# Kernel optimization log

Hardware: AMD Instinct MI355X
Metric: run time of the kernel (lower is better)

Reference implementation:

```python
import jax, jax.numpy as jnp
import numpy as np

ALPHA = 0.2      # LeakyReLU negative slope
NEG = -9e15     # mask fill value, as in pyGAT

B, N, NFEAT, NHID, NCLASS, NHEADS = 4, 2048, 128, 64, 32, 8


def setup_inputs() -> dict:
    key = jax.random.key(0)
    ks = jax.random.split(key, 8)
    x = jax.random.normal(ks[0], (B, N, NFEAT), dtype=jnp.float32)
    adj = jax.random.randint(ks[1], (B, N, N), 0, 2, dtype=jnp.int32)
    W = jax.random.normal(ks[2], (NHEADS, NFEAT, NHID), dtype=jnp.float32) * 0.1
    a1 = jax.random.normal(ks[3], (NHEADS, NHID), dtype=jnp.float32) * 0.1
    a2 = jax.random.normal(ks[4], (NHEADS, NHID), dtype=jnp.float32) * 0.1
    Wo = jax.random.normal(ks[5], (NHEADS * NHID, NCLASS), dtype=jnp.float32) * 0.1
    ao1 = jax.random.normal(ks[6], (NCLASS,), dtype=jnp.float32) * 0.1
    ao2 = jax.random.normal(ks[7], (NCLASS,), dtype=jnp.float32) * 0.1
    return {"x": x, "adj": adj, "W": W, "a1": a1, "a2": a2,
            "Wo": Wo, "ao1": ao1, "ao2": ao2}


def _gat_forward(x, adj, W, a1, a2, Wo, ao1, ao2):
    mask = adj > 0  # [B, N, N]
    # --- multi-head layer (concat=True) ---
    Wh = jnp.einsum('bnf,hfd->bhnd', x, W)          # [B,H,N,nhid]
    f1 = jnp.einsum('bhnd,hd->bhn', Wh, a1)          # Wh @ a[:nhid]
    f2 = jnp.einsum('bhnd,hd->bhn', Wh, a2)          # Wh @ a[nhid:]
    e = jax.nn.leaky_relu(f1[..., :, None] + f2[..., None, :], ALPHA)
    att = jax.nn.softmax(jnp.where(mask[:, None], e, NEG), axis=-1)
    h = jax.nn.elu(jnp.einsum('bhnm,bhmd->bhnd', att, Wh))  # [B,H,N,nhid]
    # torch.cat along dim=2: [B, N, H*nhid]
    h = jnp.transpose(h, (0, 2, 1, 3)).reshape(B, N, NHEADS * NHID)
    # (dropout layers are no-ops in eval mode)
    # --- output head (concat=False, no ELU) ---
    Wh2 = jnp.einsum('bnf,fc->bnc', h, Wo)           # [B,N,nclass]
    g1 = jnp.einsum('bnc,c->bn', Wh2, ao1)
    g2 = jnp.einsum('bnc,c->bn', Wh2, ao2)
    e2 = jax.nn.leaky_relu(g1[:, :, None] + g2[:, None, :], ALPHA)
    att2 = jax.nn.softmax(jnp.where(mask, e2, NEG), axis=-1)
    return jnp.einsum('bnm,bmc->bnc', att2, Wh2)     # [B,N,nclass]


def reference(x, adj, W, a1, a2, Wo, ao1, ao2):
    return _gat_forward(x, adj, W, a1, a2, Wo, ao1, ao2)
```

## Files before the change

kernel.cpp:

```cpp
#include <hip/hip_runtime.h>


typedef short  short8  __attribute__((ext_vector_type(8)));
typedef float  float4_ __attribute__((ext_vector_type(4)));
typedef float  float2_ __attribute__((ext_vector_type(2)));
typedef unsigned int uint4_ __attribute__((ext_vector_type(4)));

#if __has_builtin(__builtin_amdgcn_exp2f)
#define EXP2(x) __builtin_amdgcn_exp2f(x)
#else
#define EXP2(x) __expf((x) * 0.69314718055994531f)
#endif
#define LOG2E 1.44269504088896340f

static __device__ __forceinline__ unsigned short f2bf(float f) {
  unsigned u = __float_as_uint(f);
  u += 0x7fffu + ((u >> 16) & 1u);
  return (unsigned short)(u >> 16);
}
static __device__ __forceinline__ unsigned pk2bf(float a, float b) {
  return (unsigned)f2bf(a) | ((unsigned)f2bf(b) << 16);
}
static __device__ __forceinline__ unsigned upack(float s) {
  return ((unsigned)f2bf(EXP2(0.2f * s)) << 16) | f2bf(EXP2(s));
}

static __device__ __forceinline__ unsigned bitm(unsigned mb, int jj) {
#if __has_builtin(__builtin_amdgcn_sbfe)
  return (unsigned)__builtin_amdgcn_sbfe((int)mb, jj, 1);
#else
  return 0u - ((mb >> jj) & 1u);
#endif
}

static __device__ __forceinline__ unsigned wmax2(unsigned w0, unsigned w1,
    unsigned m0, unsigned m1, float2_ Av, float2_ A2v) {
  float2_ lo = {__uint_as_float(w0 << 16), __uint_as_float(w1 << 16)};
  float2_ hi = {__uint_as_float(w0 & 0xFFFF0000u), __uint_as_float(w1 & 0xFFFF0000u)};
  float2_ p = Av * lo;
  float2_ n = A2v * hi;
  float2_ m = __builtin_elementwise_max(p, n);
  unsigned e0 = __float_as_uint(m.x) & m0;
  unsigned e1 = __float_as_uint(m.y) & m1;
  return __builtin_amdgcn_perm(e1, e0, 0x07060302u);
}

__global__ __launch_bounds__(256) void k_wfrag(
    const float* __restrict__ Wm, const float* __restrict__ Wo,
    short* __restrict__ Wf, short* __restrict__ WoF) {
  if (blockIdx.x < 32) {
    const int T = blockIdx.x * 256 + threadIdx.x;
    const int lane = T & 63;
    int r = T >> 6;
    const int nt = r & 3; r >>= 2;
    const int kstep = r & 3; r >>= 2;
    const int h = r;
    const int kk = kstep * 32 + (lane >> 4) * 8;
    const int n = nt * 16 + (lane & 15);
    const float* sp = Wm + h * 8192 + kk * 64 + n;
    short8 o;
    #pragma unroll
    for (int jj = 0; jj < 8; ++jj) o[jj] = (short)f2bf(sp[jj * 64]);
    *(short8*)(Wf + T * 8) = o;
  } else {
    const int T = (blockIdx.x - 32) * 256 + threadIdx.x;
    const int lane = T & 63;
    const int nt = (T >> 6) & 1, kstep = T >> 7;
    const int kk = kstep * 32 + (lane >> 4) * 8;
    const int n = nt * 16 + (lane & 15);
    short8 o;
    #pragma unroll
    for (int jj = 0; jj < 8; ++jj) o[jj] = (short)f2bf(Wo[(kk + jj) * 32 + n]);
    *(short8*)(WoF + T * 8) = o;
  }
}

__global__ __launch_bounds__(256) void k_front(
    const int* __restrict__ adj, unsigned long long* __restrict__ maskb,
    const float* __restrict__ x, const short* __restrict__ Wf,
    const float* __restrict__ a1, const float* __restrict__ a2,
    short* __restrict__ WhF, float* __restrict__ f1, unsigned* __restrict__ f2p) {
  __shared__ float wsm[64 * 68];
  const int bx = blockIdx.x;
  const int t = threadIdx.x;
  if (bx >= 1024) {
    const int lane = t & 63, wid = t >> 6;
    const int s = lane & 15;
    const long long row0 = (long long)(bx - 1024) * 4;
    for (int rr = 0; rr < 4; ++rr) {
      const long long row = row0 + rr;
      const int4* src = (const int4*)(adj + row * 2048);
      #pragma unroll
      for (int c = 0; c < 2; ++c) {
        int4 v = src[c * 256 + t];
        unsigned nib = (v.x != 0 ? 1u : 0u) | (v.y != 0 ? 2u : 0u) |
                       (v.z != 0 ? 4u : 0u) | (v.w != 0 ? 8u : 0u);
        unsigned lo = (s < 8) ? (nib << (s * 4)) : 0u;
        unsigned hi = (s >= 8) ? (nib << ((s - 8) * 4)) : 0u;
        #pragma unroll
        for (int off = 1; off < 16; off <<= 1) {
          lo |= __shfl_xor(lo, off);
          hi |= __shfl_xor(hi, off);
        }
        if (s == 0) {
          int word = c * 16 + wid * 4 + (lane >> 4);
          maskb[row * 32 + word] = ((unsigned long long)hi << 32) | (unsigned long long)lo;
        }
      }
    }
    return;
  }
  const int itile = bx & 31, bh = bx >> 5;
  const int b = bh >> 3, h = bh & 7;
  const int i0 = itile * 64;
  const int lane = t & 63, w = t >> 6;
  const int cl = lane & 15, q = lane >> 4;
  const float* xrow = x + ((long long)b * 2048 + i0 + w * 16 + cl) * 128;
  const short* wfh = Wf + h * 8192;
  float4_ acc0 = {0.f, 0.f, 0.f, 0.f}, acc1 = acc0, acc2 = acc0, acc3 = acc0;
  #pragma unroll
  for (int kstep = 0; kstep < 4; ++kstep) {
    const float* xp = xrow + kstep * 32 + q * 8;
    const float4 xa = *(const float4*)xp;
    const float4 xb = *(const float4*)(xp + 4);
    uint4_ ap;
    ap.x = pk2bf(xa.x, xa.y);
    ap.y = pk2bf(xa.z, xa.w);
    ap.z = pk2bf(xb.x, xb.y);
    ap.w = pk2bf(xb.z, xb.w);
    const short8 af = __builtin_bit_cast(short8, ap);
    const short* bp = wfh + kstep * 2048 + lane * 8;
    const short8 b0 = *(const short8*)(bp);
    const short8 b1 = *(const short8*)(bp + 512);
    const short8 b2 = *(const short8*)(bp + 1024);
    const short8 b3 = *(const short8*)(bp + 1536);
    acc0 = __builtin_amdgcn_mfma_f32_16x16x32_bf16(af, b0, acc0, 0, 0, 0);
    acc1 = __builtin_amdgcn_mfma_f32_16x16x32_bf16(af, b1, acc1, 0, 0, 0);
    acc2 = __builtin_amdgcn_mfma_f32_16x16x32_bf16(af, b2, acc2, 0, 0, 0);
    acc3 = __builtin_amdgcn_mfma_f32_16x16x32_bf16(af, b3, acc3, 0, 0, 0);
  }
  {
    float4_ accs[4] = {acc0, acc1, acc2, acc3};
    #pragma unroll
    for (int nt = 0; nt < 4; ++nt)
      #pragma unroll
      for (int reg = 0; reg < 4; ++reg)
        wsm[(w * 16 + q * 4 + reg) * 68 + nt * 16 + cl] = accs[nt][reg];
  }
  __syncthreads();
  {
    const int row = t >> 2, seg = t & 3;
    const float* wr = wsm + row * 68 + seg * 16;
    const float4* a1p = (const float4*)(a1 + h * 64 + seg * 16);
    const float4* a2p = (const float4*)(a2 + h * 64 + seg * 16);
    float p1 = 0.f, p2 = 0.f;
    #pragma unroll
    for (int u = 0; u < 4; ++u) {
      const float4 wv = *(const float4*)(wr + u * 4);
      const float4 v1 = a1p[u];
      const float4 v2 = a2p[u];
      p1 += wv.x * v1.x + wv.y * v1.y + wv.z * v1.z + wv.w * v1.w;
      p2 += wv.x * v2.x + wv.y * v2.y + wv.z * v2.z + wv.w * v2.w;
    }
    p1 += __shfl_xor(p1, 1); p1 += __shfl_xor(p1, 2);
    p2 += __shfl_xor(p2, 1); p2 += __shfl_xor(p2, 2);
    if (seg == 0) {
      f1[(long long)bh * 2048 + i0 + row] = p1 * LOG2E;
      f2p[(long long)bh * 2048 + i0 + row] = upack(p2 * LOG2E);
    }
  }
  #pragma unroll
  for (int u = 0; u < 2; ++u) {
    const int idx = u * 256 + t;
    const int l2 = idx & 63, nt2 = (idx >> 6) & 3, ks2 = idx >> 8;
    const int jrow = ks2 * 32 + (l2 >> 4) * 8;
    const int d = nt2 * 16 + (l2 & 15);
    short8 o;
    #pragma unroll
    for (int jj = 0; jj < 8; ++jj) o[jj] = (short)f2bf(wsm[(jrow + jj) * 68 + d]);
    const long long off = (long long)bh * 131072 + (long long)itile * 4096 +
                          ks2 * 2048 + nt2 * 512 + l2 * 8;
    *(short8*)(WhF + off) = o;
  }
}

__global__ __launch_bounds__(256) void k_attn1(
    const short* __restrict__ whf, const float* __restrict__ f1v,
    const unsigned* __restrict__ f2pv, const unsigned long long* __restrict__ maskb,
    short* __restrict__ hA) {
  __shared__ short bsm[2][8192];
  __shared__ unsigned f2s[2048];
  const int bh = blockIdx.y, b = bh >> 3, hh = bh & 7;
  const int t = threadIdx.x;
  const int lane = t & 63, wid = t >> 6;
  const int cl = lane & 15, q = lane >> 4;
  const long long i_g = (long long)blockIdx.x * 64 + wid * 16 + cl;
  const float f1i = f1v[(long long)bh * 2048 + i_g];
  const float A = EXP2(f1i), A2 = EXP2(0.2f * f1i);
  const float2_ Av = {A, A}, A2v = {A2, A2};
  const uint2* mpp = (const uint2*)(maskb + ((long long)b * 2048 + i_g) * 32);
  const unsigned* f2b = f2pv + (long long)bh * 2048;
  const short* whfb = whf + (long long)bh * 131072;
  const float4* gB = (const float4*)whfb;
  const short8 vones = {16256, 16256, 16256, 16256, 16256, 16256, 16256, 16256};
  ((uint4_*)f2s)[t] = ((const uint4_*)f2b)[t];
  ((uint4_*)f2s)[256 + t] = ((const uint4_*)f2b)[256 + t];
  {
    float4 st0[4];
    #pragma unroll
    for (int u = 0; u < 4; ++u) st0[u] = gB[u * 256 + t];
    #pragma unroll
    for (int u = 0; u < 4; ++u) ((float4*)bsm[0])[u * 256 + t] = st0[u];
  }
  uint2 mw0_c = mpp[0], mw1_c = mpp[1];
  float4_ acc0 = {0.f, 0.f, 0.f, 0.f}, acc1 = acc0, acc2 = acc0, acc3 = acc0;
  float4_ accz = acc0;
  const int qs = q * 8;
  for (int s = 0; s < 16; ++s) {
    float4 stn0, stn1, stn2, stn3;
    if (s < 15) {
      const float4* gp = gB + (s + 1) * 1024 + t;
      stn0 = gp[0]; stn1 = gp[256]; stn2 = gp[512]; stn3 = gp[768];
    }
    const uint2 mwA = mw0_c, mwB = mw1_c;
    if (s < 15) { mw0_c = mpp[s * 2 + 2]; mw1_c = mpp[s * 2 + 3]; }
    __syncthreads();
    const short* bsb = bsm[s & 1] + lane * 8;
    #pragma unroll
    for (int jc2 = 0; jc2 < 2; ++jc2) {
      const int jc = s * 2 + jc2;
      const uint2 mw = jc2 ? mwB : mwA;
      #pragma unroll
      for (int ks = 0; ks < 2; ++ks) {
        const unsigned mb = (ks ? mw.y : mw.x) >> qs;
        const unsigned* up = f2s + jc * 64 + ks * 32 + qs;
        const uint4_ wa = *(const uint4_*)up;
        const uint4_ wb = *(const uint4_*)(up + 4);
        uint4_ pk;
        pk.x = wmax2(wa.x, wa.y, bitm(mb, 0), bitm(mb, 1), Av, A2v);
        pk.y = wmax2(wa.z, wa.w, bitm(mb, 2), bitm(mb, 3), Av, A2v);
        pk.z = wmax2(wb.x, wb.y, bitm(mb, 4), bitm(mb, 5), Av, A2v);
        pk.w = wmax2(wb.z, wb.w, bitm(mb, 6), bitm(mb, 7), Av, A2v);
        const short8 af = __builtin_bit_cast(short8, pk);
        const short* bp = bsb + (jc2 * 2 + ks) * 2048;
        short8 b0 = *(const short8*)(bp);
        short8 b1 = *(const short8*)(bp + 512);
        short8 b2 = *(const short8*)(bp + 1024);
        short8 b3 = *(const short8*)(bp + 1536);
        acc0 = __builtin_amdgcn_mfma_f32_16x16x32_bf16(af, b0, acc0, 0, 0, 0);
        acc1 = __builtin_amdgcn_mfma_f32_16x16x32_bf16(af, b1, acc1, 0, 0, 0);
        acc2 = __builtin_amdgcn_mfma_f32_16x16x32_bf16(af, b2, acc2, 0, 0, 0);
        acc3 = __builtin_amdgcn_mfma_f32_16x16x32_bf16(af, b3, acc3, 0, 0, 0);
        accz = __builtin_amdgcn_mfma_f32_16x16x32_bf16(af, vones, accz, 0, 0, 0);
      }
    }
    if (s < 15) {
      float4* dp = (float4*)bsm[(s + 1) & 1] + t;
      dp[0] = stn0; dp[256] = stn1; dp[512] = stn2; dp[768] = stn3;
    }
  }
  __syncthreads();
  float* hs = (float*)bsm;
  {
    float4_ accs[4] = {acc0, acc1, acc2, acc3};
    #pragma unroll
    for (int reg = 0; reg < 4; ++reg) {
      const float rz = 1.f / accz[reg];
      #pragma unroll
      for (int nt = 0; nt < 4; ++nt) {
        float v = accs[nt][reg] * rz;
        v = (v > 0.f) ? v : (__expf(v) - 1.f);
        hs[(wid * 16 + q * 4 + reg) * 68 + nt * 16 + cl] = v;
      }
    }
  }
  __syncthreads();
  const int rtg0 = b * 128 + blockIdx.x * 4;
  #pragma unroll
  for (int u = 0; u < 2; ++u) {
    const int id = u * 256 + t;
    const int l2 = id & 63, ks2 = (id >> 6) & 1, rtile = id >> 7;
    const int rowl = rtile * 16 + (l2 & 15);
    const int d = ks2 * 32 + (l2 >> 4) * 8;
    const float* hp = hs + rowl * 68 + d;
    const float4 va = *(const float4*)hp;
    const float4 vb = *(const float4*)(hp + 4);
    uint4_ o;
    o.x = pk2bf(va.x, va.y); o.y = pk2bf(va.z, va.w);
    o.z = pk2bf(vb.x, vb.y); o.w = pk2bf(vb.z, vb.w);
    const long long rt = rtg0 + rtile;
    const int kstep = hh * 2 + ks2;
    *(uint4_*)(hA + ((rt * 16 + kstep) * 64 + l2) * 8) = o;
  }
}

__global__ __launch_bounds__(128) void k_ogemm(
    const short* __restrict__ hA, const short* __restrict__ WoF,
    const float* __restrict__ ao1, const float* __restrict__ ao2,
    short* __restrict__ Wh2F, float* __restrict__ g1, unsigned* __restrict__ g2p) {
  __shared__ float w2s[32 * 36];
  const int t = threadIdx.x, lane = t & 63, wv = t >> 6;
  const int cl = lane & 15, q = lane >> 4;
  const long long rt = (long long)blockIdx.x * 2 + wv;
  float4_ acc0 = {0.f, 0.f, 0.f, 0.f}, acc1 = acc0;
  const short* ap = hA + rt * 8192 + lane * 8;
  const short* bp = WoF + lane * 8;
  #pragma unroll
  for (int kstep = 0; kstep < 16; ++kstep) {
    const short8 af = *(const short8*)(ap + kstep * 512);
    const short8 b0 = *(const short8*)(bp + kstep * 1024);
    const short8 b1 = *(const short8*)(bp + kstep * 1024 + 512);
    acc0 = __builtin_amdgcn_mfma_f32_16x16x32_bf16(af, b0, acc0, 0, 0, 0);
    acc1 = __builtin_amdgcn_mfma_f32_16x16x32_bf16(af, b1, acc1, 0, 0, 0);
  }
  const float o1a = ao1[cl], o1b = ao1[cl + 16];
  const float o2a = ao2[cl], o2b = ao2[cl + 16];
  #pragma unroll
  for (int reg = 0; reg < 4; ++reg) {
    const int rowl = wv * 16 + q * 4 + reg;
    w2s[rowl * 36 + cl] = acc0[reg];
    w2s[rowl * 36 + 16 + cl] = acc1[reg];
    float p1 = acc0[reg] * o1a + acc1[reg] * o1b;
    float p2 = acc0[reg] * o2a + acc1[reg] * o2b;
    p1 += __shfl_xor(p1, 1); p1 += __shfl_xor(p1, 2);
    p1 += __shfl_xor(p1, 4); p1 += __shfl_xor(p1, 8);
    p2 += __shfl_xor(p2, 1); p2 += __shfl_xor(p2, 2);
    p2 += __shfl_xor(p2, 4); p2 += __shfl_xor(p2, 8);
    if (cl == 0) {
      const long long row = (long long)blockIdx.x * 32 + rowl;
      g1[row] = p1 * LOG2E;
      g2p[row] = upack(p2 * LOG2E);
    }
  }
  __syncthreads();
  {
    const int l2 = t & 63, nt2 = t >> 6;
    const int g = blockIdx.x >> 6, jc = (blockIdx.x >> 1) & 31, ks2 = blockIdx.x & 1;
    const int kb = (l2 >> 4) * 8, n = nt2 * 16 + (l2 & 15);
    short8 o;
    #pragma unroll
    for (int jj = 0; jj < 8; ++jj) o[jj] = (short)f2bf(w2s[(kb + jj) * 36 + n]);
    const long long off = (long long)g * 65536 + jc * 2048 + ks2 * 1024 +
                          nt2 * 512 + l2 * 8;
    *(short8*)(Wh2F + off) = o;
  }
}

__global__ __launch_bounds__(256) void k_attn2(
    const short* __restrict__ whf2, const float* __restrict__ g1v,
    const unsigned* __restrict__ g2pv, const unsigned long long* __restrict__ maskb,
    float* __restrict__ outp) {
  __shared__ float accs[4][16][33];
  __shared__ float zsh[64];
  const int b = blockIdx.y;
  const long long i0 = (long long)blockIdx.x * 16;
  const int t = threadIdx.x, lane = t & 63, wid = t >> 6;
  const int cl = lane & 15, q = lane >> 4;
  const float g1i = g1v[(long long)b * 2048 + i0 + cl];
  const float A = EXP2(g1i), A2 = EXP2(0.2f * g1i);
  const float2_ Av = {A, A}, A2v = {A2, A2};
  const uint2* mpp = (const uint2*)(maskb + ((long long)b * 2048 + i0 + cl) * 32);
  const unsigned* g2b = g2pv + (long long)b * 2048;
  const short* wb = whf2 + (long long)b * 65536;
  const short8 vones = {16256, 16256, 16256, 16256, 16256, 16256, 16256, 16256};
  float4_ acc0 = {0.f, 0.f, 0.f, 0.f}, acc1 = acc0, accz = acc0;
  const int qs = q * 8;
  const int jc0 = wid * 8;
  uint2 mw_c = mpp[jc0];
  uint4_ wa0_c = *(const uint4_*)(g2b + jc0 * 64 + qs);
  uint4_ wb0_c = *(const uint4_*)(g2b + jc0 * 64 + qs + 4);
  uint4_ wa1_c = *(const uint4_*)(g2b + jc0 * 64 + 32 + qs);
  uint4_ wb1_c = *(const uint4_*)(g2b + jc0 * 64 + 36 + qs);
  for (int c8 = 0; c8 < 8; ++c8) {
    const int jc = jc0 + c8;
    const uint2 mw = mw_c;
    const uint4_ wa0 = wa0_c, wb0 = wb0_c, wa1 = wa1_c, wb1 = wb1_c;
    {
      const int jn = jc + ((c8 < 7) ? 1 : 0);
      const unsigned* fp = g2b + jn * 64 + qs;
      mw_c = mpp[jn];
      wa0_c = *(const uint4_*)fp;
      wb0_c = *(const uint4_*)(fp + 4);
      wa1_c = *(const uint4_*)(fp + 32);
      wb1_c = *(const uint4_*)(fp + 36);
    }
    const short* bb = wb + (jc * 2) * 1024 + lane * 8;
    {
      const unsigned mb = mw.x >> qs;
      uint4_ pk;
      pk.x = wmax2(wa0.x, wa0.y, bitm(mb, 0), bitm(mb, 1), Av, A2v);
      pk.y = wmax2(wa0.z, wa0.w, bitm(mb, 2), bitm(mb, 3), Av, A2v);
      pk.z = wmax2(wb0.x, wb0.y, bitm(mb, 4), bitm(mb, 5), Av, A2v);
      pk.w = wmax2(wb0.z, wb0.w, bitm(mb, 6), bitm(mb, 7), Av, A2v);
      const short8 af = __builtin_bit_cast(short8, pk);
      short8 b0 = *(const short8*)bb;
      short8 b1 = *(const short8*)(bb + 512);
      acc0 = __builtin_amdgcn_mfma_f32_16x16x32_bf16(af, b0, acc0, 0, 0, 0);
      acc1 = __builtin_amdgcn_mfma_f32_16x16x32_bf16(af, b1, acc1, 0, 0, 0);
      accz = __builtin_amdgcn_mfma_f32_16x16x32_bf16(af, vones, accz, 0, 0, 0);
    }
    {
      const unsigned mb = mw.y >> qs;
      uint4_ pk;
      pk.x = wmax2(wa1.x, wa1.y, bitm(mb, 0), bitm(mb, 1), Av, A2v);
      pk.y = wmax2(wa1.z, wa1.w, bitm(mb, 2), bitm(mb, 3), Av, A2v);
      pk.z = wmax2(wb1.x, wb1.y, bitm(mb, 4), bitm(mb, 5), Av, A2v);
      pk.w = wmax2(wb1.z, wb1.w, bitm(mb, 6), bitm(mb, 7), Av, A2v);
      const short8 af = __builtin_bit_cast(short8, pk);
      const short* bk = bb + 1024;
      short8 b0 = *(const short8*)bk;
      short8 b1 = *(const short8*)(bk + 512);
      acc0 = __builtin_amdgcn_mfma_f32_16x16x32_bf16(af, b0, acc0, 0, 0, 0);
      acc1 = __builtin_amdgcn_mfma_f32_16x16x32_bf16(af, b1, acc1, 0, 0, 0);
      accz = __builtin_amdgcn_mfma_f32_16x16x32_bf16(af, vones, accz, 0, 0, 0);
    }
  }
  if (cl == 0) {
    #pragma unroll
    for (int reg = 0; reg < 4; ++reg) zsh[wid * 16 + q * 4 + reg] = accz[reg];
  }
  float4_ a01[2] = {acc0, acc1};
  #pragma unroll
  for (int nt = 0; nt < 2; ++nt)
    #pragma unroll
    for (int reg = 0; reg < 4; ++reg)
      accs[wid][q * 4 + reg][nt * 16 + cl] = a01[nt][reg];
  __syncthreads();
  #pragma unroll
  for (int r = 0; r < 2; ++r) {
    int o = r * 256 + t;
    int il = o >> 5, c = o & 31;
    float s = accs[0][il][c] + accs[1][il][c] + accs[2][il][c] + accs[3][il][c];
    float Z = zsh[il] + zsh[16 + il] + zsh[32 + il] + zsh[48 + il];
    outp[((long long)b * 2048 + i0 + il) * 32 + c] = s / Z;
  }
}

extern "C" void kernel_launch(void* const* d_in, const int* in_sizes, int n_in,
                              void* d_out, int out_size, void* d_ws, size_t ws_size,
                              hipStream_t stream) {
  const float* x   = (const float*)d_in[0];
  const int*   adj = (const int*)d_in[1];
  const float* W   = (const float*)d_in[2];
  const float* a1  = (const float*)d_in[3];
  const float* a2  = (const float*)d_in[4];
  const float* Wo  = (const float*)d_in[5];
  const float* ao1 = (const float*)d_in[6];
  const float* ao2 = (const float*)d_in[7];
  float* out = (float*)d_out;
  char* ws = (char*)d_ws;

  unsigned long long* maskb = (unsigned long long*)(ws + 0);
  short* Wf   = (short*)(ws + 2097152);
  short* WoF  = (short*)(ws + 2228224);
  short* WhF  = (short*)(ws + 18874368);
  float* f1   = (float*)(ws + 27262976);
  unsigned* f2p = (unsigned*)(ws + 27525120);
  short* hA   = (short*)(ws + 27787264);
  short* Wh2F = (short*)(ws + 45613056);
  float* g1   = (float*)(ws + 46137344);
  unsigned* g2p = (unsigned*)(ws + 46170112);

  hipLaunchKernelGGL(k_wfrag, dim3(40), dim3(256), 0, stream, W, Wo, Wf, WoF);
  hipLaunchKernelGGL(k_front, dim3(3072), dim3(256), 0, stream, adj, maskb,
                     x, Wf, a1, a2, WhF, f1, f2p);
  hipLaunchKernelGGL(k_attn1, dim3(32, 32), dim3(256), 0, stream, WhF, f1, f2p, maskb, hA);
  hipLaunchKernelGGL(k_ogemm, dim3(256), dim3(128), 0, stream, hA, WoF, ao1, ao2,
                     Wh2F, g1, g2p);
  hipLaunchKernelGGL(k_attn2, dim3(128, 4), dim3(256), 0, stream, Wh2F, g1, g2p, maskb, out);
}
```

Baseline: 181.0 us.

## Switch attention layer-1 to 32x32x16 MFMA with split-K across wave pairs

Rewrites k_attn1 so each wave computes a 32-row tile with 32x32x16 bf16 MFMAs instead of 16x16x32. Waves are split into two row groups and two key halves, and the partial sums are reduced through shared memory. The WhF fragment layout and the f2 exponent storage (now separate U/U2 bf16 arrays) are changed to match the new operand layout. ELU and normalization move into the final pack stage. This cuts the MFMA count and the row-sum overhead per output, at the cost of an extra LDS reduction and sync.

```diff
diff --git a/kernel.cpp b/kernel.cpp
--- a/kernel.cpp
+++ b/kernel.cpp
@@ -4,6 +4,7 @@
 typedef short  short8  __attribute__((ext_vector_type(8)));
 typedef float  float4_ __attribute__((ext_vector_type(4)));
 typedef float  float2_ __attribute__((ext_vector_type(2)));
+typedef float  float16_ __attribute__((ext_vector_type(16)));
 typedef unsigned int uint4_ __attribute__((ext_vector_type(4)));
 
 #if __has_builtin(__builtin_amdgcn_exp2f)
@@ -39,6 +40,18 @@
   float2_ hi = {__uint_as_float(w0 & 0xFFFF0000u), __uint_as_float(w1 & 0xFFFF0000u)};
   float2_ p = Av * lo;
   float2_ n = A2v * hi;
+  float2_ m = __builtin_elementwise_max(p, n);
+  unsigned e0 = __float_as_uint(m.x) & m0;
+  unsigned e1 = __float_as_uint(m.y) & m1;
+  return __builtin_amdgcn_perm(e1, e0, 0x07060302u);
+}
+
+static __device__ __forceinline__ unsigned wmax2u(unsigned uw, unsigned u2w,
+    unsigned m0, unsigned m1, float2_ Av, float2_ A2v) {
+  float2_ Uf  = {__uint_as_float(uw << 16),  __uint_as_float(uw & 0xFFFF0000u)};
+  float2_ U2f = {__uint_as_float(u2w << 16), __uint_as_float(u2w & 0xFFFF0000u)};
+  float2_ p = Av * Uf;
+  float2_ n = A2v * U2f;
   float2_ m = __builtin_elementwise_max(p, n);
   unsigned e0 = __float_as_uint(m.x) & m0;
   unsigned e1 = __float_as_uint(m.y) & m1;
@@ -79,7 +92,8 @@
     const int* __restrict__ adj, unsigned long long* __restrict__ maskb,
     const float* __restrict__ x, const short* __restrict__ Wf,
     const float* __restrict__ a1, const float* __restrict__ a2,
-    short* __restrict__ WhF, float* __restrict__ f1, unsigned* __restrict__ f2p) {
+    short* __restrict__ WhF, float* __restrict__ f1,
+    unsigned short* __restrict__ Uv, unsigned short* __restrict__ U2v) {
   __shared__ float wsm[64 * 68];
   const int bx = blockIdx.x;
   const int t = threadIdx.x;
@@ -166,45 +180,46 @@
     p2 += __shfl_xor(p2, 1); p2 += __shfl_xor(p2, 2);
     if (seg == 0) {
       f1[(long long)bh * 2048 + i0 + row] = p1 * LOG2E;
-      f2p[(long long)bh * 2048 + i0 + row] = upack(p2 * LOG2E);
+      const float s2 = p2 * LOG2E;
+      Uv[(long long)bh * 2048 + i0 + row] = f2bf(EXP2(s2));
+      U2v[(long long)bh * 2048 + i0 + row] = f2bf(EXP2(0.2f * s2));
     }
   }
   #pragma unroll
   for (int u = 0; u < 2; ++u) {
     const int idx = u * 256 + t;
-    const int l2 = idx & 63, nt2 = (idx >> 6) & 3, ks2 = idx >> 8;
-    const int jrow = ks2 * 32 + (l2 >> 4) * 8;
-    const int d = nt2 * 16 + (l2 & 15);
+    const int l2 = idx & 63, dtile = (idx >> 6) & 1, win = (idx >> 7) & 1, ks2 = idx >> 8;
+    const int jloc = ks2 * 32 + win * 16 + (l2 >> 5) * 8;
+    const int d = dtile * 32 + (l2 & 31);
     short8 o;
     #pragma unroll
-    for (int jj = 0; jj < 8; ++jj) o[jj] = (short)f2bf(wsm[(jrow + jj) * 68 + d]);
+    for (int jj = 0; jj < 8; ++jj) o[jj] = (short)f2bf(wsm[(jloc + jj) * 68 + d]);
     const long long off = (long long)bh * 131072 + (long long)itile * 4096 +
-                          ks2 * 2048 + nt2 * 512 + l2 * 8;
+                          ks2 * 2048 + win * 1024 + dtile * 512 + l2 * 8;
     *(short8*)(WhF + off) = o;
   }
 }
 
 __global__ __launch_bounds__(256) void k_attn1(
     const short* __restrict__ whf, const float* __restrict__ f1v,
-    const unsigned* __restrict__ f2pv, const unsigned long long* __restrict__ maskb,
-    short* __restrict__ hA) {
+    const unsigned short* __restrict__ Uv, const unsigned short* __restrict__ U2v,
+    const unsigned* __restrict__ mask32, short* __restrict__ hA) {
   __shared__ short bsm[2][8192];
-  __shared__ unsigned f2s[2048];
+  __shared__ unsigned short Us[2048], U2s[2048];
   const int bh = blockIdx.y, b = bh >> 3, hh = bh & 7;
-  const int t = threadIdx.x;
-  const int lane = t & 63, wid = t >> 6;
-  const int cl = lane & 15, q = lane >> 4;
-  const long long i_g = (long long)blockIdx.x * 64 + wid * 16 + cl;
+  const int t = threadIdx.x, lane = t & 63, wid = t >> 6;
+  const int rg = wid & 1, jh = wid >> 1;
+  const int m = lane & 31, hi8 = lane >> 5;
+  const long long i_g = (long long)blockIdx.x * 64 + rg * 32 + m;
   const float f1i = f1v[(long long)bh * 2048 + i_g];
   const float A = EXP2(f1i), A2 = EXP2(0.2f * f1i);
   const float2_ Av = {A, A}, A2v = {A2, A2};
-  const uint2* mpp = (const uint2*)(maskb + ((long long)b * 2048 + i_g) * 32);
-  const unsigned* f2b = f2pv + (long long)bh * 2048;
+  const unsigned* mp = mask32 + ((long long)b * 2048 + i_g) * 64 + jh;
   const short* whfb = whf + (long long)bh * 131072;
   const float4* gB = (const float4*)whfb;
   const short8 vones = {16256, 16256, 16256, 16256, 16256, 16256, 16256, 16256};
-  ((uint4_*)f2s)[t] = ((const uint4_*)f2b)[t];
-  ((uint4_*)f2s)[256 + t] = ((const uint4_*)f2b)[256 + t];
+  ((uint4_*)Us)[t]  = ((const uint4_*)(Uv  + (long long)bh * 2048))[t];
+  ((uint4_*)U2s)[t] = ((const uint4_*)(U2v + (long long)bh * 2048))[t];
   {
     float4 st0[4];
     #pragma unroll
@@ -212,46 +227,41 @@
     #pragma unroll
     for (int u = 0; u < 4; ++u) ((float4*)bsm[0])[u * 256 + t] = st0[u];
   }
-  uint2 mw0_c = mpp[0], mw1_c = mpp[1];
-  float4_ acc0 = {0.f, 0.f, 0.f, 0.f}, acc1 = acc0, acc2 = acc0, acc3 = acc0;
-  float4_ accz = acc0;
-  const int qs = q * 8;
+  unsigned mw0_c = mp[0], mw1_c = mp[2];
+  float16_ acc0 = {0.f,0.f,0.f,0.f,0.f,0.f,0.f,0.f,0.f,0.f,0.f,0.f,0.f,0.f,0.f,0.f};
+  float16_ acc1 = acc0, accz = acc0;
+  const int uoff = jh * 32 + hi8 * 8;
   for (int s = 0; s < 16; ++s) {
     float4 stn0, stn1, stn2, stn3;
     if (s < 15) {
       const float4* gp = gB + (s + 1) * 1024 + t;
       stn0 = gp[0]; stn1 = gp[256]; stn2 = gp[512]; stn3 = gp[768];
     }
-    const uint2 mwA = mw0_c, mwB = mw1_c;
-    if (s < 15) { mw0_c = mpp[s * 2 + 2]; mw1_c = mpp[s * 2 + 3]; }
+    const unsigned mwA = mw0_c, mwB = mw1_c;
+    if (s < 15) { mw0_c = mp[(s * 2 + 2) * 2]; mw1_c = mp[(s * 2 + 3) * 2]; }
     __syncthreads();
-    const short* bsb = bsm[s & 1] + lane * 8;
+    const short* bsb = bsm[s & 1];
     #pragma unroll
     for (int jc2 = 0; jc2 < 2; ++jc2) {
       const int jc = s * 2 + jc2;
-      const uint2 mw = jc2 ? mwB : mwA;
+      const unsigned mword = jc2 ? mwB : mwA;
       #pragma unroll
-      for (int ks = 0; ks < 2; ++ks) {
-        const unsigned mb = (ks ? mw.y : mw.x) >> qs;
-        const unsigned* up = f2s + jc * 64 + ks * 32 + qs;
-        const uint4_ wa = *(const uint4_*)up;
-        const uint4_ wb = *(const uint4_*)(up + 4);
+      for (int win = 0; win < 2; ++win) {
+        const unsigned mb = mword >> (win * 16 + hi8 * 8);
+        const uint4_ uv  = *(const uint4_*)(Us  + jc * 64 + uoff + win * 16);
+        const uint4_ u2v = *(const uint4_*)(U2s + jc * 64 + uoff + win * 16);
         uint4_ pk;
-        pk.x = wmax2(wa.x, wa.y, bitm(mb, 0), bitm(mb, 1), Av, A2v);
-        pk.y = wmax2(wa.z, wa.w, bitm(mb, 2), bitm(mb, 3), Av, A2v);
-        pk.z = wmax2(wb.x, wb.y, bitm(mb, 4), bitm(mb, 5), Av, A2v);
-        pk.w = wmax2(wb.z, wb.w, bitm(mb, 6), bitm(mb, 7), Av, A2v);
+        pk.x = wmax2u(uv.x, u2v.x, bitm(mb, 0), bitm(mb, 1), Av, A2v);
+        pk.y = wmax2u(uv.y, u2v.y, bitm(mb, 2), bitm(mb, 3), Av, A2v);
+        pk.z = wmax2u(uv.z, u2v.z, bitm(mb, 4), bitm(mb, 5), Av, A2v);
+        pk.w = wmax2u(uv.w, u2v.w, bitm(mb, 6), bitm(mb, 7), Av, A2v);
         const short8 af = __builtin_bit_cast(short8, pk);
-        const short* bp = bsb + (jc2 * 2 + ks) * 2048;
-        short8 b0 = *(const short8*)(bp);
-        short8 b1 = *(const short8*)(bp + 512);
-        short8 b2 = *(const short8*)(bp + 1024);
-        short8 b3 = *(const short8*)(bp + 1536);
-        acc0 = __builtin_amdgcn_mfma_f32_16x16x32_bf16(af, b0, acc0, 0, 0, 0);
-        acc1 = __builtin_amdgcn_mfma_f32_16x16x32_bf16(af, b1, acc1, 0, 0, 0);
-        acc2 = __builtin_amdgcn_mfma_f32_16x16x32_bf16(af, b2, acc2, 0, 0, 0);
-        acc3 = __builtin_amdgcn_mfma_f32_16x16x32_bf16(af, b3, acc3, 0, 0, 0);
-        accz = __builtin_amdgcn_mfma_f32_16x16x32_bf16(af, vones, accz, 0, 0, 0);
+        const short* bp = bsb + jc2 * 4096 + jh * 2048 + win * 1024 + lane * 8;
+        const short8 b0 = *(const short8*)bp;
+        const short8 b1 = *(const short8*)(bp + 512);
+        acc0 = __builtin_amdgcn_mfma_f32_32x32x16_bf16(af, b0, acc0, 0, 0, 0);
+        acc1 = __builtin_amdgcn_mfma_f32_32x32x16_bf16(af, b1, acc1, 0, 0, 0);
+        accz = __builtin_amdgcn_mfma_f32_32x32x16_bf16(af, vones, accz, 0, 0, 0);
       }
     }
     if (s < 15) {
@@ -261,17 +271,32 @@
   }
   __syncthreads();
   float* hs = (float*)bsm;
-  {
-    float4_ accs[4] = {acc0, acc1, acc2, acc3};
-    #pragma unroll
-    for (int reg = 0; reg < 4; ++reg) {
-      const float rz = 1.f / accz[reg];
+  float* zs = hs + 64 * 68;
+  if (jh == 0) {
+    #pragma unroll
+    for (int r = 0; r < 16; ++r) {
+      const int rowl = rg * 32 + (r & 3) + 8 * (r >> 2) + 4 * hi8;
+      hs[rowl * 68 + m] = acc0[r];
+      hs[rowl * 68 + 32 + m] = acc1[r];
+    }
+    if (m == 0) {
       #pragma unroll
-      for (int nt = 0; nt < 4; ++nt) {
-        float v = accs[nt][reg] * rz;
-        v = (v > 0.f) ? v : (__expf(v) - 1.f);
-        hs[(wid * 16 + q * 4 + reg) * 68 + nt * 16 + cl] = v;
-      }
+      for (int r = 0; r < 16; ++r)
+        zs[rg * 32 + (r & 3) + 8 * (r >> 2) + 4 * hi8] = accz[r];
+    }
+  }
+  __syncthreads();
+  if (jh == 1) {
+    #pragma unroll
+    for (int r = 0; r < 16; ++r) {
+      const int rowl = rg * 32 + (r & 3) + 8 * (r >> 2) + 4 * hi8;
+      hs[rowl * 68 + m] += acc0[r];
+      hs[rowl * 68 + 32 + m] += acc1[r];
+    }
+    if (m == 0) {
+      #pragma unroll
+      for (int r = 0; r < 16; ++r)
+        zs[rg * 32 + (r & 3) + 8 * (r >> 2) + 4 * hi8] += accz[r];
     }
   }
   __syncthreads();
@@ -282,12 +307,17 @@
     const int l2 = id & 63, ks2 = (id >> 6) & 1, rtile = id >> 7;
     const int rowl = rtile * 16 + (l2 & 15);
     const int d = ks2 * 32 + (l2 >> 4) * 8;
+    const float rz = 1.f / zs[rowl];
     const float* hp = hs + rowl * 68 + d;
-    const float4 va = *(const float4*)hp;
-    const float4 vb = *(const float4*)(hp + 4);
+    float v[8];
+    #pragma unroll
+    for (int k = 0; k < 8; ++k) {
+      float x = hp[k] * rz;
+      v[k] = (x > 0.f) ? x : (__expf(x) - 1.f);
+    }
     uint4_ o;
-    o.x = pk2bf(va.x, va.y); o.y = pk2bf(va.z, va.w);
-    o.z = pk2bf(vb.x, vb.y); o.w = pk2bf(vb.z, vb.w);
+    o.x = pk2bf(v[0], v[1]); o.y = pk2bf(v[2], v[3]);
+    o.z = pk2bf(v[4], v[5]); o.w = pk2bf(v[6], v[7]);
     const long long rt = rtg0 + rtile;
     const int kstep = hh * 2 + ks2;
     *(uint4_*)(hA + ((rt * 16 + kstep) * 64 + l2) * 8) = o;
@@ -455,7 +485,8 @@
   short* WoF  = (short*)(ws + 2228224);
   short* WhF  = (short*)(ws + 18874368);
   float* f1   = (float*)(ws + 27262976);
-  unsigned* f2p = (unsigned*)(ws + 27525120);
+  unsigned short* Uv  = (unsigned short*)(ws + 27525120);
+  unsigned short* U2v = (unsigned short*)(ws + 27656192);
   short* hA   = (short*)(ws + 27787264);
   short* Wh2F = (short*)(ws + 45613056);
   float* g1   = (float*)(ws + 46137344);
@@ -463,8 +494,9 @@
 
   hipLaunchKernelGGL(k_wfrag, dim3(40), dim3(256), 0, stream, W, Wo, Wf, WoF);
   hipLaunchKernelGGL(k_front, dim3(3072), dim3(256), 0, stream, adj, maskb,
-                     x, Wf, a1, a2, WhF, f1, f2p);
-  hipLaunchKernelGGL(k_attn1, dim3(32, 32), dim3(256), 0, stream, WhF, f1, f2p, maskb, hA);
+                     x, Wf, a1, a2, WhF, f1, Uv, U2v);
+  hipLaunchKernelGGL(k_attn1, dim3(32, 32), dim3(256), 0, stream, WhF, f1, Uv, U2v,
+                     (const unsigned*)maskb, hA);
   hipLaunchKernelGGL(k_ogemm, dim3(256), dim3(128), 0, stream, hA, WoF, ao1, ao2,
                      Wh2F, g1, g2p);
   hipLaunchKernelGGL(k_attn2, dim3(128, 4), dim3(256), 0, stream, Wh2F, g1, g2p, maskb, out);
```

New measurement: 178.6 us. About the same (-1.3%).
